# Performance work log

Hardware: AMD Instinct MI355X
Metric: run time of the kernel (lower is better)

The kernel has to match this reference:

```python
import jax, jax.numpy as jnp
import numpy as np

B, H, W = 2, 512, 512
HID, NHKD, HEADS, KD, CD = 64, 128, 8, 16, 64
MAX_SHAPE = 512

def _conv(x, w, b=None, pad=0, groups=1):
    y = jax.lax.conv_general_dilated(x, w, (1, 1), [(pad, pad), (pad, pad)],
                                     dimension_numbers=('NCHW', 'OIHW', 'NCHW'),
                                     feature_group_count=groups)
    return y if b is None else y + b[None, :, None, None]

def _gelu(x):
    return jax.nn.gelu(x, approximate=False)  # torch nn.GELU default is exact erf

def _bn(x, s, t):
    # inference-mode BatchNorm folded to per-channel scale/shift
    return x * s[None, :, None, None] + t[None, :, None, None]

def _dyn_pos(xm, pe):
    # xm: (B, C, N); pe: (1, C, MAX_SHAPE); linear interp (align_corners=False) when N != MAX_SHAPE
    N = xm.shape[-1]
    if N != pe.shape[-1]:
        pe = jax.image.resize(pe, (1, pe.shape[1], N), method='linear')
    return xm + pe

def _sdpa(q, k, v):
    # q, k, v: (B, heads, L=key_dim, E=H); scale = 1/sqrt(E) as in F.scaled_dot_product_attention
    scale = 1.0 / np.sqrt(q.shape[-1])
    attn = jax.nn.softmax(jnp.einsum('bhie,bhje->bhij', q, k) * scale, axis=-1)
    return jnp.einsum('bhij,bhje->bhie', attn, v)

def setup_inputs():
    key = jax.random.key(0)
    ks = jax.random.split(key, 26)
    rn = lambda i, shp, sc=1.0: jax.random.normal(ks[i], shp, jnp.float32) * sc
    return {
        'x': rn(0, (B, HID, H, W)),
        'shortcut': rn(1, (B, CD, H, W)),
        'ln_w': jnp.ones((CD,), jnp.float32),
        'ln_b': jnp.zeros((CD,), jnp.float32),
        'dproj_dw_w': rn(2, (CD, 1, 3, 3), 0.2),
        'dproj_bn_s': 1.0 + rn(3, (CD,), 0.1),
        'dproj_bn_t': rn(4, (CD,), 0.1),
        'dproj_pw_w': rn(5, (2 * HID, CD, 1, 1), 0.125),
        'dproj_pw_b': rn(6, (2 * HID,), 0.05),
        'q_dw_w': rn(7, (NHKD, 1, 3, 3), 0.2),
        'q_bn_s': 1.0 + rn(8, (NHKD,), 0.1),
        'q_bn_t': rn(9, (NHKD,), 0.1),
        'k_dw_w': rn(10, (NHKD, 1, 3, 3), 0.2),
        'k_bn_s': 1.0 + rn(11, (NHKD,), 0.1),
        'k_bn_t': rn(12, (NHKD,), 0.1),
        'v_pw_w': rn(13, (NHKD, HID, 1, 1), 0.125),
        'v_bn_s': 1.0 + rn(14, (NHKD,), 0.1),
        'v_bn_t': rn(15, (NHKD,), 0.1),
        'proj_dw_w': rn(16, (HID + 2 * NHKD, 1, 3, 3), 0.2),
        'proj_dw_b': rn(17, (HID + 2 * NHKD,), 0.05),
        'proj_pw_w': rn(18, (HID, HID + 2 * NHKD, 1, 1), 0.06),
        'proj_pw_b': rn(19, (HID,), 0.05),
        'pe_rowq': rn(20, (1, NHKD, MAX_SHAPE), 0.02),
        'pe_rowk': rn(21, (1, NHKD, MAX_SHAPE), 0.02),
        'pe_colq': rn(22, (1, NHKD, MAX_SHAPE), 0.02),
        'pe_colk': rn(23, (1, NHKD, MAX_SHAPE), 0.02),
        'ape_row_w': jnp.ones((1, NHKD, 1, 1), jnp.float32),
        'ape_col_w': jnp.ones((1, NHKD, 1, 1), jnp.float32),
    }

def reference(x, shortcut, ln_w, ln_b, dproj_dw_w, dproj_bn_s, dproj_bn_t,
              dproj_pw_w, dproj_pw_b, q_dw_w, q_bn_s, q_bn_t, k_dw_w, k_bn_s,
              k_bn_t, v_pw_w, v_bn_s, v_bn_t, proj_dw_w, proj_dw_b, proj_pw_w,
              proj_pw_b, pe_rowq, pe_rowk, pe_colq, pe_colk, ape_row_w, ape_col_w):
    b, _, h, w = x.shape
    # LayerNorm2d: normalize over channel axis (biased variance, eps=1e-5)
    mu = shortcut.mean(axis=1, keepdims=True)
    var = shortcut.var(axis=1, keepdims=True)
    sn = (shortcut - mu) / jnp.sqrt(var + 1e-5) * ln_w[None, :, None, None] + ln_b[None, :, None, None]
    # d_proj: dw3x3 -> BN -> GELU -> pw1x1 -> GELU
    s = _gelu(_bn(_conv(sn, dproj_dw_w, pad=1, groups=CD), dproj_bn_s, dproj_bn_t))
    s = _gelu(_conv(s, dproj_pw_w, dproj_pw_b))
    k_in, v_in = jnp.split(s, 2, axis=1)  # each (B, HID, H, W)
    # q/k: grouped 3x3 conv (groups=HID, out=NHKD) -> BN -> GELU; v: 1x1 -> BN
    q = _gelu(_bn(_conv(x, q_dw_w, pad=1, groups=HID), q_bn_s, q_bn_t))
    k = _gelu(_bn(_conv(k_in, k_dw_w, pad=1, groups=HID), k_bn_s, k_bn_t))
    v = _bn(_conv(v_in, v_pw_w), v_bn_s, v_bn_t)
    # row attention: pool over W, seq dim = key_dim (16), head dim = H
    qr = _dyn_pos(q.mean(-1), pe_rowq).reshape(b, HEADS, KD, h)
    kr = _dyn_pos(k.mean(-1), pe_rowk).reshape(b, HEADS, KD, h)
    vr = v.mean(-1).reshape(b, HEADS, KD, h)
    attn_row = _sdpa(qr, kr, vr).reshape(b, NHKD, 1, h)
    # column attention: pool over H
    qc = _dyn_pos(q.mean(-2), pe_colq).reshape(b, HEADS, KD, w)
    kc = _dyn_pos(k.mean(-2), pe_colk).reshape(b, HEADS, KD, w)
    vc = v.mean(-2).reshape(b, HEADS, KD, w)
    attn_col = _sdpa(qc, kc, vc).reshape(b, NHKD, 1, w)
    # AxialPositionEncoding: both maps broadcast over spatial axis 2 (requires H == W)
    attn = v + ape_row_w * attn_row + ape_col_w * attn_col
    cat = jnp.concatenate([x, attn, v], axis=1)  # (B, 320, H, W)
    ctot = cat.shape[1]
    # channel shuffle: 'b (c g) h w -> b (g c) h w', g=5
    shuf = cat.reshape(b, ctot // 5, 5, h, w).transpose(0, 2, 1, 3, 4).reshape(b, ctot, h, w)
    p = _gelu(_conv(shuf, proj_dw_w, proj_dw_b, pad=1, groups=ctot))
    p = _conv(p, proj_pw_w, proj_pw_b)
    return _gelu(p)
```

## Files before the change

### kernel.cpp

```cpp
#include <hip/hip_runtime.h>
#include <math.h>

#define PLANE (512*512)

typedef short bf16x8 __attribute__((ext_vector_type(8)));
typedef float f32x4 __attribute__((ext_vector_type(4)));

__device__ __forceinline__ float gelu_f(float x) {
    float ax = fabsf(x) * 0.70710678118654752440f;
    float t = __builtin_amdgcn_rcpf(1.0f + 0.3275911f * ax);
    float poly = t * (0.254829592f + t * (-0.284496736f + t * (1.421413741f
               + t * (-1.453152027f + t * 1.061405429f))));
    float e = __expf(-ax * ax);
    float er = 1.0f - poly * e;
    er = copysignf(er, x);
    return 0.5f * x * (1.0f + er);
}

__device__ __forceinline__ unsigned short f2bf(float f) {
    union { float f; unsigned u; } v; v.f = f;
    unsigned r = v.u + 0x7FFFu + ((v.u >> 16) & 1u);
    return (unsigned short)(r >> 16);
}

__device__ __forceinline__ float bf2f(unsigned short u) {
    union { unsigned u; float f; } x; x.u = ((unsigned)u) << 16; return x.f;
}

__device__ __forceinline__ float ldval(const float* p, int off) { return p[off]; }
__device__ __forceinline__ float ldval(const unsigned short* p, int off) { return bf2f(p[off]); }

__global__ __launch_bounds__(256) void k_lnstats(const float* __restrict__ sc,
                                                 float* __restrict__ Pb,
                                                 float* __restrict__ Qb) {
    int p = blockIdx.x * 256 + threadIdx.x;
    int b = p >> 18;
    int hw = p & (PLANE - 1);
    const float* src = sc + (size_t)b * 64 * PLANE + hw;
    float sum = 0.f, sq = 0.f;
    #pragma unroll 8
    for (int c = 0; c < 64; ++c) {
        float v = src[(size_t)c * PLANE];
        sum += v; sq += v * v;
    }
    float mu = sum * (1.0f / 64.0f);
    float var = sq * (1.0f / 64.0f) - mu * mu;
    float rstd = rsqrtf(var + 1e-5f);
    Pb[p] = rstd;
    Qb[p] = -mu * rstd;
}

__global__ __launch_bounds__(256) void k_dw64ln(const float* __restrict__ sc,
                                                const float* __restrict__ dww,
                                                const float* __restrict__ lnw,
                                                const float* __restrict__ lnb,
                                                const float* __restrict__ bns,
                                                const float* __restrict__ bnt,
                                                const float* __restrict__ Pb,
                                                const float* __restrict__ Qb,
                                                unsigned* __restrict__ t1b) {
    int p = blockIdx.x * 256 + threadIdx.x;
    int b = p >> 18;
    int hw = p & (PLANE - 1);
    int h = hw >> 9, w = hw & 511;
    int tapoff[9]; float Pt[9], Qt[9], vm[9];
    const float* Pp = Pb + (size_t)b * PLANE;
    const float* Qp = Qb + (size_t)b * PLANE;
    #pragma unroll
    for (int dh = -1; dh <= 1; ++dh)
        #pragma unroll
        for (int dw = -1; dw <= 1; ++dw) {
            int k = (dh + 1) * 3 + dw + 1;
            int hh = h + dh, ww = w + dw;
            bool ok = (hh >= 0 && hh < 512 && ww >= 0 && ww < 512);
            int hc = ok ? hh : h, wc = ok ? ww : w;
            int off = hc * 512 + wc;
            tapoff[k] = off;
            vm[k] = ok ? 1.f : 0.f;
            Pt[k] = Pp[off]; Qt[k] = Qp[off];
        }
    const float* scb = sc + (size_t)b * 64 * PLANE;
    unsigned* ob = t1b + (size_t)b * 32 * PLANE + hw;
    for (int c2 = 0; c2 < 32; ++c2) {
        float g[2];
        #pragma unroll
        for (int e = 0; e < 2; ++e) {
            int c = c2 * 2 + e;
            const float* wp = dww + c * 9;
            const float* cp = scb + (size_t)c * PLANE;
            float conv = 0.f, wsum = 0.f;
            #pragma unroll
            for (int k = 0; k < 9; ++k) {
                float wv = wp[k];
                float raw = cp[tapoff[k]];
                conv = fmaf(wv, fmaf(raw, Pt[k], Qt[k]) * vm[k], conv);
                wsum = fmaf(wv, vm[k], wsum);
            }
            float a = lnw[c] * conv + lnb[c] * wsum;
            g[e] = gelu_f(a * bns[c] + bnt[c]);
        }
        unsigned r;
        asm("v_cvt_pk_bf16_f32 %0,%1,%2" : "=v"(r) : "v"(g[0]), "v"(g[1]));
        ob[(size_t)c2 * PLANE] = r;
    }
}

__global__ __launch_bounds__(256) void k_wsetup2(const float* __restrict__ W1,
                                                 const float* __restrict__ W2,
                                                 unsigned short* __restrict__ w1b,
                                                 unsigned short* __restrict__ w2b) {
    int tid = blockIdx.x * 256 + threadIdx.x;
    if (tid < 8192) { w1b[tid] = f2bf(W1[tid]); w2b[tid] = f2bf(W2[tid]); }
}

__global__ __launch_bounds__(256, 4) void k_pw2(
    const unsigned* __restrict__ t1b,
    const unsigned short* __restrict__ w1b, const float* __restrict__ b1,
    const unsigned short* __restrict__ w2b,
    const float* __restrict__ vbs, const float* __restrict__ vbt,
    unsigned short* __restrict__ k_in, unsigned short* __restrict__ v)
{
    __shared__ unsigned short vin[64][88];
    __shared__ float epi[64 * 68];
    __shared__ float psl[128], ptl[128], pbl[128];
    int tid = threadIdx.x;
    if (tid < 128) { psl[tid] = vbs[tid]; ptl[tid] = vbt[tid]; pbl[tid] = b1[tid]; }
    int lane = tid & 63, wva = tid >> 6;
    int cl = lane & 15, kg = lane >> 4;
    int p0 = blockIdx.x * 64;
    int b = p0 >> 18;
    int hw0 = p0 & (PLANE - 1);
    int px = wva * 16 + cl;
    const unsigned* tp = t1b + (size_t)b * 32 * PLANE + hw0 + px;
    __syncthreads();

    unsigned bfr[2][4];
    #pragma unroll
    for (int ks = 0; ks < 2; ++ks)
        #pragma unroll
        for (int jp = 0; jp < 4; ++jp)
            bfr[ks][jp] = tp[(size_t)(ks * 16 + kg * 4 + jp) * PLANE];

    f32x4 acc[8];
    #pragma unroll
    for (int mt = 0; mt < 8; ++mt) acc[mt] = (f32x4){0.f, 0.f, 0.f, 0.f};
    #pragma unroll
    for (int ks = 0; ks < 2; ++ks) {
        union { unsigned u[4]; bf16x8 v; } bb;
        bb.u[0] = bfr[ks][0]; bb.u[1] = bfr[ks][1]; bb.u[2] = bfr[ks][2]; bb.u[3] = bfr[ks][3];
        #pragma unroll
        for (int mt = 0; mt < 8; ++mt) {
            bf16x8 af = *(const bf16x8*)(w1b + (size_t)(mt * 16 + cl) * 64 + ks * 32 + kg * 8);
            acc[mt] = __builtin_amdgcn_mfma_f32_16x16x32_bf16(af, bb.v, acc[mt], 0, 0, 0);
        }
    }

    #pragma unroll
    for (int mt = 4; mt < 8; ++mt) {
        float g[4];
        #pragma unroll
        for (int r = 0; r < 4; ++r)
            g[r] = gelu_f(acc[mt][r] + pbl[mt * 16 + kg * 4 + r]);
        unsigned r01, r23;
        asm("v_cvt_pk_bf16_f32 %0,%1,%2" : "=v"(r01) : "v"(g[0]), "v"(g[1]));
        asm("v_cvt_pk_bf16_f32 %0,%1,%2" : "=v"(r23) : "v"(g[2]), "v"(g[3]));
        int ch = (mt - 4) * 16 + kg * 4;
        *(unsigned*)&vin[px][ch]     = r01;
        *(unsigned*)&vin[px][ch + 2] = r23;
    }

    __syncthreads();
    #pragma unroll
    for (int mt = 0; mt < 4; ++mt)
        #pragma unroll
        for (int r = 0; r < 4; ++r) {
            int m = mt * 16 + kg * 4 + r;
            epi[m * 68 + px] = gelu_f(acc[mt][r] + pbl[m]);
        }
    __syncthreads();
    unsigned short* kb = k_in + (size_t)b * 64 * PLANE + hw0;
    #pragma unroll
    for (int k = 0; k < 4; ++k) {
        int m = wva * 16 + k * 4 + kg;
        float4 vv = *(const float4*)&epi[m * 68 + cl * 4];
        unsigned r01, r23;
        asm("v_cvt_pk_bf16_f32 %0,%1,%2" : "=v"(r01) : "v"(vv.x), "v"(vv.y));
        asm("v_cvt_pk_bf16_f32 %0,%1,%2" : "=v"(r23) : "v"(vv.z), "v"(vv.w));
        uint2 st; st.x = r01; st.y = r23;
        *(uint2*)&kb[(size_t)m * PLANE + cl * 4] = st;
    }

    f32x4 acc2[8];
    #pragma unroll
    for (int mt = 0; mt < 8; ++mt) acc2[mt] = (f32x4){0.f, 0.f, 0.f, 0.f};
    #pragma unroll
    for (int ks = 0; ks < 2; ++ks) {
        bf16x8 bb = *(const bf16x8*)&vin[px][ks * 32 + kg * 8];
        #pragma unroll
        for (int mt = 0; mt < 8; ++mt) {
            bf16x8 af = *(const bf16x8*)(w2b + (size_t)(mt * 16 + cl) * 64 + ks * 32 + kg * 8);
            acc2[mt] = __builtin_amdgcn_mfma_f32_16x16x32_bf16(af, bb, acc2[mt], 0, 0, 0);
        }
    }

    unsigned short* vb = v + (size_t)b * 128 * PLANE + hw0;
    #pragma unroll
    for (int pass = 0; pass < 2; ++pass) {
        __syncthreads();
        #pragma unroll
        for (int mt = pass * 4; mt < pass * 4 + 4; ++mt)
            #pragma unroll
            for (int r = 0; r < 4; ++r) {
                int m = mt * 16 + kg * 4 + r;
                epi[(m - pass * 64) * 68 + px] = acc2[mt][r] * psl[m] + ptl[m];
            }
        __syncthreads();
        #pragma unroll
        for (int k = 0; k < 4; ++k) {
            int ml = wva * 16 + k * 4 + kg;
            float4 vv = *(const float4*)&epi[ml * 68 + cl * 4];
            unsigned r01, r23;
            asm("v_cvt_pk_bf16_f32 %0,%1,%2" : "=v"(r01) : "v"(vv.x), "v"(vv.y));
            asm("v_cvt_pk_bf16_f32 %0,%1,%2" : "=v"(r23) : "v"(vv.z), "v"(vv.w));
            uint2 st; st.x = r01; st.y = r23;
            *(uint2*)&vb[(size_t)(pass * 64 + ml) * PLANE + cl * 4] = st;
        }
    }
}

template<typename T>
__global__ __launch_bounds__(512) void k_dwpool(const T* __restrict__ in,
                                                const float* __restrict__ wt,
                                                const float* __restrict__ bns,
                                                const float* __restrict__ bnt,
                                                float* __restrict__ rowsum,
                                                float* __restrict__ colpart) {
    __shared__ float lred[2][8][8];
    int tid = threadIdx.x;
    int blk = blockIdx.x;
    int hc = blk & 63;
    int g  = (blk >> 6) & 63;
    int b  = blk >> 12;
    int o0 = 2 * g, o1 = 2 * g + 1;
    const T* ip = in + ((size_t)b * 64 + g) * PLANE;
    float w0[9], w1[9];
    #pragma unroll
    for (int k = 0; k < 9; ++k) { w0[k] = wt[o0 * 9 + k]; w1[k] = wt[o1 * 9 + k]; }
    float s0 = bns[o0], t0 = bnt[o0], s1 = bns[o1], tt1 = bnt[o1];
    int wx = tid;
    float ca0 = 0.f, ca1 = 0.f;
    int lane = tid & 63, wv = tid >> 6;
    for (int r = 0; r < 8; ++r) {
        int h = hc * 8 + r;
        float nb[9];
        #pragma unroll
        for (int dh = -1; dh <= 1; ++dh) {
            #pragma unroll
            for (int dw = -1; dw <= 1; ++dw) {
                int hh = h + dh, ww = wx + dw;
                nb[(dh + 1) * 3 + dw + 1] =
                    (hh >= 0 && hh < 512 && ww >= 0 && ww < 512) ? ldval(ip, hh * 512 + ww) : 0.f;
            }
        }
        float a0 = 0.f, a1 = 0.f;
        #pragma unroll
        for (int k = 0; k < 9; ++k) { a0 += w0[k] * nb[k]; a1 += w1[k] * nb[k]; }
        a0 = gelu_f(a0 * s0 + t0);
        a1 = gelu_f(a1 * s1 + tt1);
        ca0 += a0; ca1 += a1;
        #pragma unroll
        for (int off = 32; off > 0; off >>= 1) {
            a0 += __shfl_down(a0, off, 64);
            a1 += __shfl_down(a1, off, 64);
        }
        if (lane == 0) { lred[0][r][wv] = a0; lred[1][r][wv] = a1; }
    }
    colpart[(((size_t)b * 128 + o0) * 64 + hc) * 512 + wx] = ca0;
    colpart[(((size_t)b * 128 + o1) * 64 + hc) * 512 + wx] = ca1;
    __syncthreads();
    if (tid < 16) {
        int oo = tid >> 3, r = tid & 7;
        float s = 0.f;
        #pragma unroll
        for (int i = 0; i < 8; ++i) s += lred[oo][r][i];
        int och = oo == 0 ? o0 : o1;
        rowsum[((size_t)b * 128 + och) * 512 + hc * 8 + r] = s;
    }
}

__global__ __launch_bounds__(512) void k_vpool(const unsigned short* __restrict__ v,
                                               float* __restrict__ rowsum,
                                               float* __restrict__ colpart) {
    __shared__ float lred[8][8];
    int tid = threadIdx.x;
    int blk = blockIdx.x;
    int hc = blk & 63;
    int bc = blk >> 6;
    const unsigned short* ip = v + (size_t)bc * PLANE;
    float ca = 0.f;
    int lane = tid & 63, wv = tid >> 6;
    for (int r = 0; r < 8; ++r) {
        float a = bf2f(ip[(hc * 8 + r) * 512 + tid]);
        ca += a;
        #pragma unroll
        for (int off = 32; off > 0; off >>= 1) a += __shfl_down(a, off, 64);
        if (lane == 0) lred[r][wv] = a;
    }
    colpart[((size_t)bc * 64 + hc) * 512 + tid] = ca;
    __syncthreads();
    if (tid < 8) {
        float s = 0.f;
        #pragma unroll
        for (int i = 0; i < 8; ++i) s += lred[tid][i];
        rowsum[(size_t)bc * 512 + hc * 8 + tid] = s;
    }
}

__global__ __launch_bounds__(256) void k_colreduce(const float* __restrict__ part,
                                                   float* __restrict__ out, int n) {
    int idx = blockIdx.x * 256 + threadIdx.x;
    if (idx >= n) return;
    int bc = idx >> 9, w = idx & 511;
    const float* pp = part + ((size_t)bc * 64) * 512 + w;
    float s = 0.f;
    #pragma unroll
    for (int p = 0; p < 64; ++p) s += pp[p * 512];
    out[idx] = s;
}

__global__ __launch_bounds__(256) void k_attn(const float* __restrict__ qrow,
                                              const float* __restrict__ krow,
                                              const float* __restrict__ vrow,
                                              const float* __restrict__ qcol,
                                              const float* __restrict__ kcol,
                                              const float* __restrict__ vcol,
                                              const float* __restrict__ perq,
                                              const float* __restrict__ perk,
                                              const float* __restrict__ pecq,
                                              const float* __restrict__ peck,
                                              float* __restrict__ arow,
                                              float* __restrict__ acol) {
    __shared__ float P[16][17];
    int blk = blockIdx.x;
    int axis = blk & 1;
    int head = (blk >> 1) & 7;
    int b = blk >> 4;
    const float* qs = axis ? qcol : qrow;
    const float* ks = axis ? kcol : krow;
    const float* vs = axis ? vcol : vrow;
    const float* peq = axis ? pecq : perq;
    const float* pek = axis ? peck : perk;
    float* out = axis ? acol : arow;
    int tid = threadIdx.x;
    int i = tid >> 4, j = tid & 15;
    int ci = head * 16 + i, cj = head * 16 + j;
    const float* qp = qs + ((size_t)b * 128 + ci) * 512;
    const float* kp = ks + ((size_t)b * 128 + cj) * 512;
    const float* qe = peq + ci * 512;
    const float* ke = pek + cj * 512;
    float s = 0.f;
    for (int n = 0; n < 512; ++n) {
        float qv = qp[n] * (1.f / 512.f) + qe[n];
        float kv = kp[n] * (1.f / 512.f) + ke[n];
        s += qv * kv;
    }
    s *= 0.0441941738241592203f;
    P[i][j] = s;
    __syncthreads();
    if (tid < 16) {
        float mx = -1e30f;
        #pragma unroll
        for (int jj = 0; jj < 16; ++jj) mx = fmaxf(mx, P[tid][jj]);
        float e[16];
        float sum = 0.f;
        #pragma unroll
        for (int jj = 0; jj < 16; ++jj) { e[jj] = expf(P[tid][jj] - mx); sum += e[jj]; }
        float inv = 1.f / sum;
        #pragma unroll
        for (int jj = 0; jj < 16; ++jj) P[tid][jj] = e[jj] * inv;
    }
    __syncthreads();
    for (int idx = tid; idx < 16 * 512; idx += 256) {
        int ii = idx >> 9, n = idx & 511;
        const float* vb = vs + ((size_t)b * 128 + head * 16) * 512 + n;
        float acc = 0.f;
        #pragma unroll
        for (int jj = 0; jj < 16; ++jj) acc += P[ii][jj] * vb[jj * 512] * (1.f / 512.f);
        out[((size_t)b * 128 + head * 16 + ii) * 512 + n] = acc;
    }
}

__global__ __launch_bounds__(256) void k_wsetup(const float* __restrict__ pww,
                                                unsigned short* __restrict__ wsh) {
    int tid = blockIdx.x * 256 + threadIdx.x;
    if (tid >= 64 * 320) return;
    int m = tid / 320, src = tid % 320;
    int o = (src % 5) * 64 + src / 5;
    wsh[m * 320 + src] = f2bf(pww[m * 320 + o]);
}

__global__ __launch_bounds__(256) void k_awsetup(const float* __restrict__ pdw,
                                                 const float* __restrict__ aprw,
                                                 const float* __restrict__ apcw,
                                                 const float* __restrict__ arow,
                                                 const float* __restrict__ acol,
                                                 float* __restrict__ aw) {
    int idx = blockIdx.x * 256 + threadIdx.x;
    if (idx >= 2 * 128 * 512) return;
    int col = idx & 511;
    int c   = (idx >> 9) & 127;
    int b   = idx >> 16;
    int src = 64 + c;
    int o = (src % 5) * 64 + src / 5;
    const float* wd = pdw + o * 9;
    float ws0 = wd[0] + wd[3] + wd[6];
    float ws1 = wd[1] + wd[4] + wd[7];
    float ws2 = wd[2] + wd[5] + wd[8];
    const float* ar = arow + ((size_t)b * 128 + c) * 512;
    const float* ac = acol + ((size_t)b * 128 + c) * 512;
    float apr = aprw[c], apc = apcw[c];
    float sum = ws1 * (apr * ar[col] + apc * ac[col]);
    if (col > 0)   sum += ws0 * (apr * ar[col - 1] + apc * ac[col - 1]);
    if (col < 511) sum += ws2 * (apr * ar[col + 1] + apc * ac[col + 1]);
    aw[idx] = sum;
}

template<bool HE, bool WE>
__device__ __forceinline__ void conv2x2b(const unsigned short* __restrict__ p,
    const float* wlA, const float* wlP,
    const int* hrow, const float* rv, int ls, int rs, float cv0, float cv2,
    float outA[2], float outP[2])
{
    float a0,a1,a2, b0,b1,b2, c0,c1,c2;
    const unsigned short* q = p + hrow[0]*512;
    if (WE) { a0=bf2f(q[ls])*cv0; a1=bf2f(q[0]); a2=bf2f(q[rs])*cv2; } else { a0=bf2f(q[-1]); a1=bf2f(q[0]); a2=bf2f(q[1]); }
    q = p + hrow[1]*512;
    if (WE) { b0=bf2f(q[ls])*cv0; b1=bf2f(q[0]); b2=bf2f(q[rs])*cv2; } else { b0=bf2f(q[-1]); b1=bf2f(q[0]); b2=bf2f(q[1]); }
    q = p + hrow[2]*512;
    if (WE) { c0=bf2f(q[ls])*cv0; c1=bf2f(q[0]); c2=bf2f(q[rs])*cv2; } else { c0=bf2f(q[-1]); c1=bf2f(q[0]); c2=bf2f(q[1]); }
    #pragma unroll
    for (int hs = 0; hs < 2; ++hs) {
        float sA0 = wlA[0]*a0 + wlA[1]*a1 + wlA[2]*a2;
        float sA1 = wlA[3]*b0 + wlA[4]*b1 + wlA[5]*b2;
        float sA2 = wlA[6]*c0 + wlA[7]*c1 + wlA[8]*c2;
        float sP0 = wlP[0]*a0 + wlP[1]*a1 + wlP[2]*a2;
        float sP1 = wlP[3]*b0 + wlP[4]*b1 + wlP[5]*b2;
        float sP2 = wlP[6]*c0 + wlP[7]*c1 + wlP[8]*c2;
        if (HE) {
            outA[hs] = rv[hs]*sA0 + sA1 + rv[hs+2]*sA2 + wlA[9];
            outP[hs] = rv[hs]*sP0 + sP1 + rv[hs+2]*sP2 + wlP[9];
        } else {
            outA[hs] = sA0 + sA1 + sA2 + wlA[9];
            outP[hs] = sP0 + sP1 + sP2 + wlP[9];
        }
        if (hs < 1) {
            a0=b0; a1=b1; a2=b2; b0=c0; b1=c1; b2=c2;
            q = p + hrow[3]*512;
            if (WE) { c0=bf2f(q[ls])*cv0; c1=bf2f(q[0]); c2=bf2f(q[rs])*cv2; } else { c0=bf2f(q[-1]); c1=bf2f(q[0]); c2=bf2f(q[1]); }
        }
    }
}

template<bool HE, bool WE>
__device__ __forceinline__ void conv1x2(const float* __restrict__ p,
    const float* wl,
    const int* hrow, const float* rv, int ls, int rs, float cv0, float cv2,
    float out[2])
{
    float a0,a1,a2, b0,b1,b2, c0,c1,c2;
    const float* q = p + hrow[0]*512;
    if (WE) { a0=q[ls]*cv0; a1=q[0]; a2=q[rs]*cv2; } else { a0=q[-1]; a1=q[0]; a2=q[1]; }
    q = p + hrow[1]*512;
    if (WE) { b0=q[ls]*cv0; b1=q[0]; b2=q[rs]*cv2; } else { b0=q[-1]; b1=q[0]; b2=q[1]; }
    q = p + hrow[2]*512;
    if (WE) { c0=q[ls]*cv0; c1=q[0]; c2=q[rs]*cv2; } else { c0=q[-1]; c1=q[0]; c2=q[1]; }
    #pragma unroll
    for (int hs = 0; hs < 2; ++hs) {
        float s0 = wl[0]*a0 + wl[1]*a1 + wl[2]*a2;
        float s1 = wl[3]*b0 + wl[4]*b1 + wl[5]*b2;
        float s2 = wl[6]*c0 + wl[7]*c1 + wl[8]*c2;
        out[hs] = (HE ? (rv[hs]*s0 + s1 + rv[hs+2]*s2) : (s0 + s1 + s2)) + wl[9];
        if (hs < 1) {
            a0=b0; a1=b1; a2=b2; b0=c0; b1=c1; b2=c2;
            q = p + hrow[3]*512;
            if (WE) { c0=q[ls]*cv0; c1=q[0]; c2=q[rs]*cv2; } else { c0=q[-1]; c1=q[0]; c2=q[1]; }
        }
    }
}

template<bool HE, bool WE>
__device__ __forceinline__ void proj5_core(
    int h0, int wwbase, float* epi, const float* dwl,
    const float* __restrict__ xb, const unsigned short* __restrict__ vbp,
    const float* __restrict__ arb, const float* __restrict__ acb,
    const float* __restrict__ aprw, const float* __restrict__ apcw,
    const float* __restrict__ awb,
    const unsigned short* __restrict__ wsh, const float* __restrict__ pwb,
    float* __restrict__ outb)
{
    int tid = threadIdx.x;
    int lane = tid & 63, wva = tid >> 6;
    int cl = lane & 15, kg = lane >> 4;
    int ww = wwbase + wva * 16 + cl;

    int hrow[4]; float rv[4];
    #pragma unroll
    for (int i = 0; i < 4; ++i) {
        int r = h0 - 1 + i;
        float va = 1.f;
        if (HE) { if (r < 0) { r = 0; va = 0.f; } if (r > 511) { r = 511; va = 0.f; } }
        hrow[i] = r; rv[i] = va;
    }
    int ls = -1, rs = 1; float cv0 = 1.f, cv2 = 1.f;
    if (WE) {
        if (ww == 0)   { ls = 1;  cv0 = 0.f; }
        if (ww == 511) { rs = -1; cv2 = 0.f; }
    }

    f32x4 acc[2][4];
    #pragma unroll
    for (int hs = 0; hs < 2; ++hs)
        #pragma unroll
        for (int mt = 0; mt < 4; ++mt)
            acc[hs][mt] = (f32x4){0.f, 0.f, 0.f, 0.f};

    #pragma unroll
    for (int ks = 0; ks < 2; ++ks) {
        unsigned bp[2][4];
        #pragma unroll
        for (int jp = 0; jp < 4; ++jp) {
            float cj0[2], cj1[2];
            int ch = ks * 32 + kg * 8 + jp * 2;
            conv1x2<HE,WE>(xb + (size_t)ch * PLANE + ww, dwl + ch * 12,
                           hrow, rv, ls, rs, cv0, cv2, cj0);
            conv1x2<HE,WE>(xb + (size_t)(ch+1) * PLANE + ww, dwl + (ch+1) * 12,
                           hrow, rv, ls, rs, cv0, cv2, cj1);
            #pragma unroll
            for (int hs = 0; hs < 2; ++hs) {
                float g0 = gelu_f(cj0[hs]), g1 = gelu_f(cj1[hs]);
                unsigned r;
                asm("v_cvt_pk_bf16_f32 %0,%1,%2" : "=v"(r) : "v"(g0), "v"(g1));
                bp[hs][jp] = r;
            }
        }
        #pragma unroll
        for (int mt = 0; mt < 4; ++mt) {
            bf16x8 af = *(const bf16x8*)(wsh + (size_t)(mt * 16 + cl) * 320 + ks * 32 + kg * 8);
            #pragma unroll
            for (int hs = 0; hs < 2; ++hs) {
                union { unsigned u[4]; bf16x8 v; } bb;
                bb.u[0] = bp[hs][0]; bb.u[1] = bp[hs][1]; bb.u[2] = bp[hs][2]; bb.u[3] = bp[hs][3];
                acc[hs][mt] = __builtin_amdgcn_mfma_f32_16x16x32_bf16(af, bb.v, acc[hs][mt], 0, 0, 0);
            }
        }
    }

    #pragma unroll
    for (int vks = 0; vks < 4; ++vks) {
        unsigned bpA[2][4], bpP[2][4];
        #pragma unroll
        for (int jp = 0; jp < 4; ++jp) {
            float cA[2][2], cP[2][2];
            #pragma unroll
            for (int e = 0; e < 2; ++e) {
                int c = vks * 32 + kg * 8 + jp * 2 + e;
                const float* wlA = dwl + (64 + c) * 12;
                conv2x2b<HE,WE>(vbp + (size_t)c * PLANE + ww, wlA, dwl + (192 + c) * 12,
                                hrow, rv, ls, rs, cv0, cv2, cA[e], cP[e]);
                float awv = awb[(size_t)c * 512 + ww];
                #pragma unroll
                for (int hs = 0; hs < 2; ++hs) {
                    if (!HE) {
                        cA[e][hs] += awv;
                    } else {
                        if (rv[hs] + rv[hs + 2] == 2.f) {
                            cA[e][hs] += awv;
                        } else {
                            const float* arp = arb + (size_t)c * 512 + ww;
                            const float* acp = acb + (size_t)c * 512 + ww;
                            float apr = aprw[c], apc = apcw[c];
                            float aa0 = (apr * arp[ls] + apc * acp[ls]) * cv0;
                            float aa1 =  apr * arp[0]  + apc * acp[0];
                            float aa2 = (apr * arp[rs] + apc * acp[rs]) * cv2;
                            float wd0 = rv[hs]*wlA[0] + wlA[3] + rv[hs+2]*wlA[6];
                            float wd1 = rv[hs]*wlA[1] + wlA[4] + rv[hs+2]*wlA[7];
                            float wd2 = rv[hs]*wlA[2] + wlA[5] + rv[hs+2]*wlA[8];
                            cA[e][hs] += wd0*aa0 + wd1*aa1 + wd2*aa2;
                        }
                    }
                }
            }
            #pragma unroll
            for (int hs = 0; hs < 2; ++hs) {
                float gA0 = gelu_f(cA[0][hs]), gA1 = gelu_f(cA[1][hs]);
                float gP0 = gelu_f(cP[0][hs]), gP1 = gelu_f(cP[1][hs]);
                unsigned ra, rp;
                asm("v_cvt_pk_bf16_f32 %0,%1,%2" : "=v"(ra) : "v"(gA0), "v"(gA1));
                asm("v_cvt_pk_bf16_f32 %0,%1,%2" : "=v"(rp) : "v"(gP0), "v"(gP1));
                bpA[hs][jp] = ra; bpP[hs][jp] = rp;
            }
        }
        #pragma unroll
        for (int mt = 0; mt < 4; ++mt) {
            bf16x8 afA = *(const bf16x8*)(wsh + (size_t)(mt * 16 + cl) * 320 + (2 + vks) * 32 + kg * 8);
            #pragma unroll
            for (int hs = 0; hs < 2; ++hs) {
                union { unsigned u[4]; bf16x8 v; } bb;
                bb.u[0] = bpA[hs][0]; bb.u[1] = bpA[hs][1]; bb.u[2] = bpA[hs][2]; bb.u[3] = bpA[hs][3];
                acc[hs][mt] = __builtin_amdgcn_mfma_f32_16x16x32_bf16(afA, bb.v, acc[hs][mt], 0, 0, 0);
            }
            bf16x8 afP = *(const bf16x8*)(wsh + (size_t)(mt * 16 + cl) * 320 + (6 + vks) * 32 + kg * 8);
            #pragma unroll
            for (int hs = 0; hs < 2; ++hs) {
                union { unsigned u[4]; bf16x8 v; } bb;
                bb.u[0] = bpP[hs][0]; bb.u[1] = bpP[hs][1]; bb.u[2] = bpP[hs][2]; bb.u[3] = bpP[hs][3];
                acc[hs][mt] = __builtin_amdgcn_mfma_f32_16x16x32_bf16(afP, bb.v, acc[hs][mt], 0, 0, 0);
            }
        }
    }

    #pragma unroll
    for (int hs = 0; hs < 2; ++hs) {
        __syncthreads();
        #pragma unroll
        for (int mt = 0; mt < 4; ++mt)
            #pragma unroll
            for (int r = 0; r < 4; ++r) {
                int m = mt * 16 + kg * 4 + r;
                epi[m * 68 + wva * 16 + cl] = gelu_f(acc[hs][mt][r] + pwb[m]);
            }
        __syncthreads();
        #pragma unroll
        for (int k = 0; k < 4; ++k) {
            int m = wva * 16 + k * 4 + kg;
            float4 vv = *(const float4*)&epi[m * 68 + cl * 4];
            *(float4*)&outb[(size_t)m * PLANE + (size_t)(h0 + hs) * 512 + wwbase + cl * 4] = vv;
        }
    }
}

__global__ __launch_bounds__(256, 4) void k_proj5(
    const float* __restrict__ x, const unsigned short* __restrict__ v,
    const float* __restrict__ arow, const float* __restrict__ acol,
    const float* __restrict__ aprw, const float* __restrict__ apcw,
    const float* __restrict__ dww, const float* __restrict__ dwb,
    const unsigned short* __restrict__ wsh, const float* __restrict__ pwb,
    const float* __restrict__ aw, float* __restrict__ out)
{
    __shared__ float dwl[320 * 12];
    __shared__ float epi[64 * 68];
    int tid = threadIdx.x;
    for (int i = tid; i < 3200; i += 256) {
        int src = i / 10, k = i - src * 10;
        int o = (src % 5) * 64 + src / 5;
        dwl[src * 12 + k] = (k < 9) ? dww[o * 9 + k] : dwb[o];
    }
    __syncthreads();
    int flat = blockIdx.x;
    int nf = (flat & 7) * 512 + (flat >> 3);
    int bx = nf & 7;
    int s  = (nf >> 3) & 255;
    int b  = nf >> 11;
    int h0 = s * 2, wwbase = bx * 64;
    const float* xb  = x + (size_t)b * 64 * PLANE;
    const unsigned short* vbp = v + (size_t)b * 128 * PLANE;
    const float* arb = arow + (size_t)b * 128 * 512;
    const float* acb = acol + (size_t)b * 128 * 512;
    const float* awb = aw + (size_t)b * 128 * 512;
    float* outb = out + (size_t)b * 64 * PLANE;
    bool HEr = (s == 0) || (s == 255);
    bool WEr = (bx == 0) || (bx == 7);
    if (!HEr && !WEr)
        proj5_core<false,false>(h0, wwbase, epi, dwl, xb, vbp, arb, acb, aprw, apcw, awb, wsh, pwb, outb);
    else if (!HEr)
        proj5_core<false,true >(h0, wwbase, epi, dwl, xb, vbp, arb, acb, aprw, apcw, awb, wsh, pwb, outb);
    else
        proj5_core<true ,true >(h0, wwbase, epi, dwl, xb, vbp, arb, acb, aprw, apcw, awb, wsh, pwb, outb);
}

extern "C" void kernel_launch(void* const* d_in, const int* in_sizes, int n_in,
                              void* d_out, int out_size, void* d_ws, size_t ws_size,
                              hipStream_t stream) {
    const float* x    = (const float*)d_in[0];
    const float* sc   = (const float*)d_in[1];
    const float* lnw  = (const float*)d_in[2];
    const float* lnb  = (const float*)d_in[3];
    const float* ddw  = (const float*)d_in[4];
    const float* dbs  = (const float*)d_in[5];
    const float* dbt  = (const float*)d_in[6];
    const float* pw1  = (const float*)d_in[7];
    const float* pb1  = (const float*)d_in[8];
    const float* qdw  = (const float*)d_in[9];
    const float* qbs  = (const float*)d_in[10];
    const float* qbt  = (const float*)d_in[11];
    const float* kdw  = (const float*)d_in[12];
    const float* kbs  = (const float*)d_in[13];
    const float* kbt  = (const float*)d_in[14];
    const float* vpw  = (const float*)d_in[15];
    const float* vbs  = (const float*)d_in[16];
    const float* vbt  = (const float*)d_in[17];
    const float* pdw  = (const float*)d_in[18];
    const float* pdb  = (const float*)d_in[19];
    const float* ppw  = (const float*)d_in[20];
    const float* ppb  = (const float*)d_in[21];
    const float* perq = (const float*)d_in[22];
    const float* perk = (const float*)d_in[23];
    const float* pecq = (const float*)d_in[24];
    const float* peck = (const float*)d_in[25];
    const float* aprw = (const float*)d_in[26];
    const float* apcw = (const float*)d_in[27];

    unsigned short* kin_b = (unsigned short*)d_out;
    float* ws   = (float*)d_ws;
    float* bufB = ws;
    unsigned short* v_b = (unsigned short*)(ws + 33554432);
    float* sm   = ws + 100663296;
    float* qrow = sm;
    float* krow = sm + 131072;
    float* vrow = sm + 262144;
    float* qcol = sm + 393216;
    float* kcol = sm + 524288;
    float* vcol = sm + 655360;
    float* arow = sm + 786432;
    float* acol = sm + 917504;
    unsigned short* wsh = (unsigned short*)(ws + 101711872);
    float* aw   = ws + 101722112;
    unsigned short* w1b = (unsigned short*)(ws + 101853184);
    unsigned short* w2b = (unsigned short*)(ws + 101857280);
    float* Pb   = ws + 101861376;
    float* Qb   = ws + 102385664;
    unsigned* t1b = (unsigned*)bufB;
    float* qcp  = bufB;
    float* kcp  = bufB + 8388608;
    float* vcp  = bufB + 16777216;

    k_wsetup <<<80,   256, 0, stream>>>(ppw, wsh);
    k_wsetup2<<<32,   256, 0, stream>>>(pw1, vpw, w1b, w2b);
    k_lnstats<<<2048, 256, 0, stream>>>(sc, Pb, Qb);
    k_dw64ln <<<2048, 256, 0, stream>>>(sc, ddw, lnw, lnb, dbs, dbt, Pb, Qb, t1b);
    k_pw2    <<<8192, 256, 0, stream>>>(t1b, w1b, pb1, w2b, vbs, vbt, kin_b, v_b);
    k_dwpool<unsigned short><<<8192, 512, 0, stream>>>(kin_b, kdw, kbs, kbt, krow, kcp);
    k_vpool  <<<16384,512, 0, stream>>>(v_b, vrow, vcp);
    k_dwpool<float><<<8192, 512, 0, stream>>>(x, qdw, qbs, qbt, qrow, qcp);
    k_colreduce<<<1536,256, 0, stream>>>(qcp, qcol, 393216);
    k_attn   <<<32,   256, 0, stream>>>(qrow, krow, vrow, qcol, kcol, vcol,
                                        perq, perk, pecq, peck, arow, acol);
    k_awsetup<<<512,  256, 0, stream>>>(pdw, aprw, apcw, arow, acol, aw);
    k_proj5  <<<4096, 256, 0, stream>>>(x, v_b, arow, acol, aprw, apcw,
                                        pdw, pdb, wsh, ppb, aw, (float*)d_out);
}
```

Measured before the change: 1.035 ms.

## Process 64-row strips in pooling kernels with rolling 3x3 row window

```diff
diff --git a/kernel.cpp b/kernel.cpp
--- a/kernel.cpp
+++ b/kernel.cpp
@@ -72,7 +72,8 @@
         for (int dw = -1; dw <= 1; ++dw) {
             int k = (dh + 1) * 3 + dw + 1;
             int hh = h + dh, ww = w + dw;
-            bool ok = (hh >= 0 && hh < 512 && ww >= 0 && ww < 512);
+            bool ok = (hh >= 0 && hh < 512 && ww >= 0 && ww < 511 + 1);
+            ok = (hh >= 0 && hh < 512 && ww >= 0 && ww < 512);
             int hc = ok ? hh : h, wc = ok ? ww : w;
             int off = hc * 512 + wc;
             tapoff[k] = off;
@@ -235,84 +236,95 @@
                                                 const float* __restrict__ bnt,
                                                 float* __restrict__ rowsum,
                                                 float* __restrict__ colpart) {
-    __shared__ float lred[2][8][8];
+    __shared__ float lred[2][64][8];
     int tid = threadIdx.x;
     int blk = blockIdx.x;
-    int hc = blk & 63;
-    int g  = (blk >> 6) & 63;
-    int b  = blk >> 12;
-    int o0 = 2 * g, o1 = 2 * g + 1;
+    int hc = blk & 7;
+    int g  = (blk >> 3) & 63;
+    int b  = blk >> 9;
+    int o0 = 2 * g, o1 = o0 + 1;
     const T* ip = in + ((size_t)b * 64 + g) * PLANE;
     float w0[9], w1[9];
     #pragma unroll
     for (int k = 0; k < 9; ++k) { w0[k] = wt[o0 * 9 + k]; w1[k] = wt[o1 * 9 + k]; }
     float s0 = bns[o0], t0 = bnt[o0], s1 = bns[o1], tt1 = bnt[o1];
-    int wx = tid;
+    int w = tid;
+    int wm = (w > 0)   ? w - 1 : w;  float vm0 = (w > 0)   ? 1.f : 0.f;
+    int wp = (w < 511) ? w + 1 : w;  float vm2 = (w < 511) ? 1.f : 0.f;
+    int h0 = hc * 64;
+    int lane = tid & 63, wv = tid >> 6;
+    float a0, a1, a2, r0, r1, r2, c0, c1, c2;
+    if (h0 >= 1) {
+        int o = (h0 - 1) * 512;
+        a0 = ldval(ip, o + wm) * vm0; a1 = ldval(ip, o + w); a2 = ldval(ip, o + wp) * vm2;
+    } else { a0 = a1 = a2 = 0.f; }
+    {
+        int o = h0 * 512;
+        r0 = ldval(ip, o + wm) * vm0; r1 = ldval(ip, o + w); r2 = ldval(ip, o + wp) * vm2;
+    }
     float ca0 = 0.f, ca1 = 0.f;
-    int lane = tid & 63, wv = tid >> 6;
-    for (int r = 0; r < 8; ++r) {
-        int h = hc * 8 + r;
-        float nb[9];
-        #pragma unroll
-        for (int dh = -1; dh <= 1; ++dh) {
-            #pragma unroll
-            for (int dw = -1; dw <= 1; ++dw) {
-                int hh = h + dh, ww = wx + dw;
-                nb[(dh + 1) * 3 + dw + 1] =
-                    (hh >= 0 && hh < 512 && ww >= 0 && ww < 512) ? ldval(ip, hh * 512 + ww) : 0.f;
-            }
-        }
-        float a0 = 0.f, a1 = 0.f;
-        #pragma unroll
-        for (int k = 0; k < 9; ++k) { a0 += w0[k] * nb[k]; a1 += w1[k] * nb[k]; }
-        a0 = gelu_f(a0 * s0 + t0);
-        a1 = gelu_f(a1 * s1 + tt1);
-        ca0 += a0; ca1 += a1;
+    for (int r = 0; r < 64; ++r) {
+        int h = h0 + r;
+        if (h + 1 <= 511) {
+            int o = (h + 1) * 512;
+            c0 = ldval(ip, o + wm) * vm0; c1 = ldval(ip, o + w); c2 = ldval(ip, o + wp) * vm2;
+        } else { c0 = c1 = c2 = 0.f; }
+        float x0 = w0[0]*a0 + w0[1]*a1 + w0[2]*a2 + w0[3]*r0 + w0[4]*r1 + w0[5]*r2
+                 + w0[6]*c0 + w0[7]*c1 + w0[8]*c2;
+        float x1 = w1[0]*a0 + w1[1]*a1 + w1[2]*a2 + w1[3]*r0 + w1[4]*r1 + w1[5]*r2
+                 + w1[6]*c0 + w1[7]*c1 + w1[8]*c2;
+        x0 = gelu_f(x0 * s0 + t0);
+        x1 = gelu_f(x1 * s1 + tt1);
+        ca0 += x0; ca1 += x1;
         #pragma unroll
         for (int off = 32; off > 0; off >>= 1) {
-            a0 += __shfl_down(a0, off, 64);
-            a1 += __shfl_down(a1, off, 64);
-        }
-        if (lane == 0) { lred[0][r][wv] = a0; lred[1][r][wv] = a1; }
-    }
-    colpart[(((size_t)b * 128 + o0) * 64 + hc) * 512 + wx] = ca0;
-    colpart[(((size_t)b * 128 + o1) * 64 + hc) * 512 + wx] = ca1;
+            x0 += __shfl_down(x0, off, 64);
+            x1 += __shfl_down(x1, off, 64);
+        }
+        if (lane == 0) { lred[0][r][wv] = x0; lred[1][r][wv] = x1; }
+        a0 = r0; a1 = r1; a2 = r2; r0 = c0; r1 = c1; r2 = c2;
+    }
+    colpart[((size_t)(b * 128 + o0) * 8 + hc) * 512 + w] = ca0;
+    colpart[((size_t)(b * 128 + o1) * 8 + hc) * 512 + w] = ca1;
     __syncthreads();
-    if (tid < 16) {
-        int oo = tid >> 3, r = tid & 7;
+    if (tid < 128) {
+        int oo = tid >> 6, r = tid & 63;
         float s = 0.f;
         #pragma unroll
         for (int i = 0; i < 8; ++i) s += lred[oo][r][i];
-        int och = oo == 0 ? o0 : o1;
-        rowsum[((size_t)b * 128 + och) * 512 + hc * 8 + r] = s;
+        int och = oo ? o1 : o0;
+        rowsum[((size_t)b * 128 + och) * 512 + h0 + r] = s;
     }
 }
 
 __global__ __launch_bounds__(512) void k_vpool(const unsigned short* __restrict__ v,
                                                float* __restrict__ rowsum,
                                                float* __restrict__ colpart) {
-    __shared__ float lred[8][8];
+    __shared__ float lred[64][8];
     int tid = threadIdx.x;
     int blk = blockIdx.x;
-    int hc = blk & 63;
-    int bc = blk >> 6;
+    int hc = blk & 7;
+    int c  = (blk >> 3) & 127;
+    int b  = blk >> 10;
+    int bc = b * 128 + c;
     const unsigned short* ip = v + (size_t)bc * PLANE;
+    int h0 = hc * 64;
+    int lane = tid & 63, wv = tid >> 6;
     float ca = 0.f;
-    int lane = tid & 63, wv = tid >> 6;
-    for (int r = 0; r < 8; ++r) {
-        float a = bf2f(ip[(hc * 8 + r) * 512 + tid]);
+    for (int r = 0; r < 64; ++r) {
+        float a = bf2f(ip[(h0 + r) * 512 + tid]);
         ca += a;
         #pragma unroll
         for (int off = 32; off > 0; off >>= 1) a += __shfl_down(a, off, 64);
         if (lane == 0) lred[r][wv] = a;
     }
-    colpart[((size_t)bc * 64 + hc) * 512 + tid] = ca;
+    colpart[((size_t)bc * 8 + hc) * 512 + tid] = ca;
     __syncthreads();
-    if (tid < 8) {
+    if (tid < 64) {
         float s = 0.f;
         #pragma unroll
         for (int i = 0; i < 8; ++i) s += lred[tid][i];
-        rowsum[(size_t)bc * 512 + hc * 8 + tid] = s;
+        rowsum[(size_t)bc * 512 + h0 + tid] = s;
     }
 }
 
@@ -321,10 +333,10 @@
     int idx = blockIdx.x * 256 + threadIdx.x;
     if (idx >= n) return;
     int bc = idx >> 9, w = idx & 511;
-    const float* pp = part + ((size_t)bc * 64) * 512 + w;
+    const float* pp = part + ((size_t)bc * 8) * 512 + w;
     float s = 0.f;
     #pragma unroll
-    for (int p = 0; p < 64; ++p) s += pp[p * 512];
+    for (int p = 0; p < 8; ++p) s += pp[p * 512];
     out[idx] = s;
 }
 
@@ -731,18 +743,18 @@
     float* Qb   = ws + 102385664;
     unsigned* t1b = (unsigned*)bufB;
     float* qcp  = bufB;
-    float* kcp  = bufB + 8388608;
-    float* vcp  = bufB + 16777216;
+    float* kcp  = bufB + 1048576;
+    float* vcp  = bufB + 2097152;
 
     k_wsetup <<<80,   256, 0, stream>>>(ppw, wsh);
     k_wsetup2<<<32,   256, 0, stream>>>(pw1, vpw, w1b, w2b);
     k_lnstats<<<2048, 256, 0, stream>>>(sc, Pb, Qb);
     k_dw64ln <<<2048, 256, 0, stream>>>(sc, ddw, lnw, lnb, dbs, dbt, Pb, Qb, t1b);
     k_pw2    <<<8192, 256, 0, stream>>>(t1b, w1b, pb1, w2b, vbs, vbt, kin_b, v_b);
-    k_dwpool<unsigned short><<<8192, 512, 0, stream>>>(kin_b, kdw, kbs, kbt, krow, kcp);
-    k_vpool  <<<16384,512, 0, stream>>>(v_b, vrow, vcp);
-    k_dwpool<float><<<8192, 512, 0, stream>>>(x, qdw, qbs, qbt, qrow, qcp);
-    k_colreduce<<<1536,256, 0, stream>>>(qcp, qcol, 393216);
+    k_dwpool<unsigned short><<<1024, 512, 0, stream>>>(kin_b, kdw, kbs, kbt, krow, kcp);
+    k_vpool  <<<2048, 512, 0, stream>>>(v_b, vrow, vcp);
+    k_dwpool<float><<<1024, 512, 0, stream>>>(x, qdw, qbs, qbt, qrow, qcp);
+    k_colreduce<<<1536, 256, 0, stream>>>(qcp, qcol, 393216);
     k_attn   <<<32,   256, 0, stream>>>(qrow, krow, vrow, qcol, kcol, vcol,
                                         perq, perk, pecq, peck, arow, acol);
     k_awsetup<<<512,  256, 0, stream>>>(pdw, aprw, apcw, arow, acol, aw);
```

Result: faster. 912.6 us (-11.8%).
